# Optimization experiments

Hardware: AMD Instinct MI355X
Metric: run time of the kernel (lower is better)

## Reference

```python
import jax, jax.numpy as jnp
import numpy as np

NUM_USERS = 80000
NUM_ITEMS = 40000
NUM_NODES = NUM_USERS + NUM_ITEMS
LATENT_DIM = 64
N_LAYERS = 3
ALPHA = 0.8
E_POS = 3_000_000
E_NEG = 1_500_000
E_PATH = 2_000_000
N_PATHS = 6


def _make_edges(rng, n_edges, n_nodes):
    # sample keys, dedupe so COO is coalesced (distinct (row,col) pairs)
    keys = rng.integers(0, n_nodes * n_nodes, size=int(n_edges * 1.05), dtype=np.int64)
    keys = np.unique(keys)[:n_edges]
    assert keys.shape[0] == n_edges
    row = (keys // n_nodes).astype(np.int32)
    col = (keys % n_nodes).astype(np.int32)
    return row, col


def setup_inputs() -> dict:
    key = jax.random.key(0)
    k1, k2, k3, k4, k5 = jax.random.split(key, 5)
    rng = np.random.default_rng(0)

    pos_row, pos_col = _make_edges(rng, E_POS, NUM_NODES)
    neg_row, neg_col = _make_edges(rng, E_NEG, NUM_NODES)
    p_row, p_col = _make_edges(rng, E_PATH, NUM_NODES)

    # path membership counts: for each coalesced edge, how many times each of the
    # 6 path matrices contains it (0/1 here); at least one path per edge
    counts = (rng.random((E_PATH, N_PATHS)) < 0.5).astype(np.float32)
    empty = counts.sum(axis=1) == 0
    counts[empty, 0] = 1.0

    return {
        "user_emb": 0.1 * jax.random.normal(k1, (NUM_USERS, LATENT_DIM), jnp.float32),
        "item_emb": 0.1 * jax.random.normal(k2, (NUM_ITEMS, LATENT_DIM), jnp.float32),
        "theta": jnp.ones((N_PATHS,), jnp.float32) / N_PATHS,
        "pos_row": jnp.asarray(pos_row),
        "pos_col": jnp.asarray(pos_col),
        "pos_val": jax.random.uniform(k3, (E_POS,), jnp.float32, 0.01, 1.0),
        "neg_row": jnp.asarray(neg_row),
        "neg_col": jnp.asarray(neg_col),
        "neg_val": jax.random.uniform(k4, (E_NEG,), jnp.float32, 0.01, 1.0),
        "p_row": jnp.asarray(p_row),
        "p_col": jnp.asarray(p_col),
        "p_counts": jnp.asarray(counts),
    }


def _spmm(row, col, val, x, n_nodes):
    # y = A @ x with A given as COO edge list: gather + segment scatter-add
    return jax.ops.segment_sum(val[:, None] * x[col], row, num_segments=n_nodes)


def reference(user_emb, item_emb, theta, pos_row, pos_col, pos_val,
              neg_row, neg_col, neg_val, p_row, p_col, p_counts):
    n = NUM_NODES

    # ---- build path-weighted matrix (coalesce + sparse row softmax, eq.(2)) ----
    theta_w = jax.nn.softmax(theta)                 # [6]
    vals = p_counts @ theta_w                       # coalesced values per edge [E_path]
    exp_v = jnp.exp(vals)
    row_sums = jax.ops.segment_sum(exp_v, p_row, num_segments=n)
    soft_v = exp_v / (row_sums[p_row] + 1e-12)      # row-level sparse softmax

    # ---- PEE: E_0 = P @ all_emb ----
    all_emb = jnp.concatenate([user_emb, item_emb], axis=0)  # [N, D]
    e = _spmm(p_row, p_col, soft_v, all_emb, n)
    embs = [e]

    # ---- signed propagation ----
    for _ in range(N_LAYERS):
        e_pos = _spmm(pos_row, pos_col, pos_val, e, n)
        e_neg_a = _spmm(neg_row, neg_col, neg_val, e, n)
        e = e_pos + ALPHA * (e - e_neg_a)
        embs.append(e)

    light_out = jnp.mean(jnp.stack(embs, axis=1), axis=1)   # [N, D]
    users = light_out[:NUM_USERS]
    items = light_out[NUM_USERS:]
    return users, items
```

## Files before the change

kernel.cpp:

```cpp
#include <hip/hip_runtime.h>

#define NUM_USERS 80000
#define NUM_ITEMS 40000
#define NUM_NODES 120000
#define DIM 64
#define ALPHA_C 0.8f

typedef unsigned short u16;
typedef unsigned int u32;

__device__ __forceinline__ u16 f2bf(float f) {
    union { float f; u32 i; } v;
    v.f = f;
    u32 i = v.i;
    u32 r = (i + 0x7FFFu + ((i >> 16) & 1u)) >> 16;
    return (u16)r;
}
__device__ __forceinline__ float lo_bf(u32 u) { return __uint_as_float(u << 16); }
__device__ __forceinline__ float hi_bf(u32 u) { return __uint_as_float(u & 0xffff0000u); }

__device__ __forceinline__ void acc8(float* __restrict__ acc, float v, uint4 q) {
    const u32* p = (const u32*)&q;
#pragma unroll
    for (int k = 0; k < 4; ++k) {
        u32 u = p[k];
        acc[2 * k]     = fmaf(v, lo_bf(u), acc[2 * k]);
        acc[2 * k + 1] = fmaf(v, hi_bf(u), acc[2 * k + 1]);
    }
}

__device__ __forceinline__ uint4 ldrow(const u16* __restrict__ x, int c, int li) {
    return *((const uint4*)(x + (size_t)c * DIM) + li);
}

__device__ __forceinline__ void seg_pipe(const int* __restrict__ col,
                                         const float* __restrict__ val,
                                         int start, int end,
                                         const u16* __restrict__ x,
                                         int li, float* __restrict__ acc) {
    int n = end - start;
    const int* cp = col + start;
    const float* vp = val + start;
    int np = n >> 1;
    if (np >= 2) {
        int   ca0 = cp[0], ca1 = cp[1];
        float va0 = vp[0], va1 = vp[1];
        int   cb0 = cp[2], cb1 = cp[3];
        float vb0 = vp[2], vb1 = vp[3];
        uint4 xa0 = ldrow(x, ca0, li);
        uint4 xa1 = ldrow(x, ca1, li);
        for (int p = 2; p < np; ++p) {
            int   cc0 = cp[2 * p],     cc1 = cp[2 * p + 1];
            float vc0 = vp[2 * p],     vc1 = vp[2 * p + 1];
            uint4 xb0 = ldrow(x, cb0, li);
            uint4 xb1 = ldrow(x, cb1, li);
            acc8(acc, va0, xa0);
            acc8(acc, va1, xa1);
            va0 = vb0; va1 = vb1; xa0 = xb0; xa1 = xb1;
            cb0 = cc0; cb1 = cc1; vb0 = vc0; vb1 = vc1;
        }
        uint4 xb0 = ldrow(x, cb0, li);
        uint4 xb1 = ldrow(x, cb1, li);
        acc8(acc, va0, xa0);
        acc8(acc, va1, xa1);
        acc8(acc, vb0, xb0);
        acc8(acc, vb1, xb1);
        if (n & 1) {
            int c = cp[n - 1];
            float v = vp[n - 1];
            uint4 xq = ldrow(x, c, li);
            acc8(acc, v, xq);
        }
    } else {
        for (int e = 0; e < n; ++e) {
            int c = cp[e];
            float v = vp[e];
            uint4 xq = ldrow(x, c, li);
            acc8(acc, v, xq);
        }
    }
}

__global__ void k_softmax_theta(const float* __restrict__ theta,
                                float* __restrict__ theta_w) {
    if (threadIdx.x == 0 && blockIdx.x == 0) {
        float m = -1e30f;
        for (int i = 0; i < 6; ++i) m = fmaxf(m, theta[i]);
        float e[6];
        float s = 0.f;
        for (int i = 0; i < 6; ++i) { e[i] = expf(theta[i] - m); s += e[i]; }
        for (int i = 0; i < 6; ++i) theta_w[i] = e[i] / s;
    }
}

__global__ void k_expv(const float* __restrict__ p_counts,
                       const float* __restrict__ theta_w,
                       float* __restrict__ exp_v, int E) {
    int i = blockIdx.x * blockDim.x + threadIdx.x;
    if (i >= E) return;
    const float* c = p_counts + (size_t)i * 6;
    float v = c[0] * theta_w[0] + c[1] * theta_w[1] + c[2] * theta_w[2] +
              c[3] * theta_w[3] + c[4] * theta_w[4] + c[5] * theta_w[5];
    exp_v[i] = expf(v);
}

__device__ __forceinline__ void lower_bound_ptr(const int* __restrict__ rows,
                                                int nnz, int r,
                                                int* __restrict__ ptr) {
    int lo = 0, hi = nnz;
    while (lo < hi) {
        int mid = (lo + hi) >> 1;
        if (rows[mid] < r) lo = mid + 1; else hi = mid;
    }
    ptr[r] = lo;
}

__global__ void k_row_ptr3(const int* __restrict__ rows_a, int nnz_a, int* __restrict__ pa,
                           const int* __restrict__ rows_b, int nnz_b, int* __restrict__ pb,
                           const int* __restrict__ rows_c, int nnz_c, int* __restrict__ pc) {
    int t = blockIdx.x * blockDim.x + threadIdx.x;
    int which = t / (NUM_NODES + 1);
    int r = t - which * (NUM_NODES + 1);
    if (which == 0) lower_bound_ptr(rows_a, nnz_a, r, pa);
    else if (which == 1) lower_bound_ptr(rows_b, nnz_b, r, pb);
    else if (which == 2) lower_bound_ptr(rows_c, nnz_c, r, pc);
}

__global__ void k_cvt(const float* __restrict__ user_emb,
                      const float* __restrict__ item_emb,
                      u16* __restrict__ emb16) {
    int i = blockIdx.x * blockDim.x + threadIdx.x;
    size_t f = (size_t)i * 4;
    const size_t UTOT = (size_t)NUM_USERS * DIM;
    const size_t TOT = (size_t)NUM_NODES * DIM;
    if (f >= TOT) return;
    float4 v = (f < UTOT) ? *(const float4*)(user_emb + f)
                          : *(const float4*)(item_emb + (f - UTOT));
    ushort4 o;
    o.x = f2bf(v.x); o.y = f2bf(v.y); o.z = f2bf(v.z); o.w = f2bf(v.w);
    *(ushort4*)(emb16 + f) = o;
}

__global__ void k_path(const u16* __restrict__ emb16,
                       const float* __restrict__ exp_v,
                       const int* __restrict__ rp,
                       const int* __restrict__ cols,
                       u16* __restrict__ e0,
                       float* __restrict__ sum_out) {
    int t = blockIdx.x * blockDim.x + threadIdx.x;
    int row = t >> 3;
    if (row >= NUM_NODES) return;
    int li = threadIdx.x & 7;
    int start = rp[row], end = rp[row + 1];

    float s = 0.f;
    for (int e = start + li; e < end; e += 8) s += exp_v[e];
    s += __shfl_xor(s, 1);
    s += __shfl_xor(s, 2);
    s += __shfl_xor(s, 4);
    float inv = 1.0f / (s + 1e-12f);

    float acc[8];
#pragma unroll
    for (int k = 0; k < 8; ++k) acc[k] = 0.f;

    seg_pipe(cols, exp_v, start, end, emb16, li, acc);

#pragma unroll
    for (int k = 0; k < 8; ++k) acc[k] *= inv;

    u32 o[4];
#pragma unroll
    for (int k = 0; k < 4; ++k)
        o[k] = (u32)f2bf(acc[2 * k]) | ((u32)f2bf(acc[2 * k + 1]) << 16);
    *((uint4*)(e0 + (size_t)row * DIM) + li) = *(uint4*)o;
    float4* sp = (float4*)(sum_out + (size_t)row * DIM) + li * 2;
    sp[0] = make_float4(acc[0], acc[1], acc[2], acc[3]);
    sp[1] = make_float4(acc[4], acc[5], acc[6], acc[7]);
}

__global__ void k_layer(const u16* __restrict__ e_in,
                        u16* __restrict__ e_out,
                        float* __restrict__ sum_io,
                        const int* __restrict__ rp_p,
                        const int* __restrict__ col_p,
                        const float* __restrict__ val_p,
                        const int* __restrict__ rp_n,
                        const int* __restrict__ col_n,
                        const float* __restrict__ val_n,
                        int is_final) {
    int t = blockIdx.x * blockDim.x + threadIdx.x;
    int row = t >> 3;
    if (row >= NUM_NODES) return;
    int li = threadIdx.x & 7;

    float accp[8], accn[8];
#pragma unroll
    for (int k = 0; k < 8; ++k) { accp[k] = 0.f; accn[k] = 0.f; }

    seg_pipe(col_p, val_p, rp_p[row], rp_p[row + 1], e_in, li, accp);
    seg_pipe(col_n, val_n, rp_n[row], rp_n[row + 1], e_in, li, accn);

    uint4 eq = *((const uint4*)(e_in + (size_t)row * DIM) + li);
    const u32* ep = (const u32*)&eq;
    float res[8];
#pragma unroll
    for (int k = 0; k < 4; ++k) {
        res[2 * k]     = accp[2 * k]     + ALPHA_C * (lo_bf(ep[k]) - accn[2 * k]);
        res[2 * k + 1] = accp[2 * k + 1] + ALPHA_C * (hi_bf(ep[k]) - accn[2 * k + 1]);
    }
    float4* sp = (float4*)(sum_io + (size_t)row * DIM) + li * 2;
    float4 s0 = sp[0], s1 = sp[1];
    s0.x += res[0]; s0.y += res[1]; s0.z += res[2]; s0.w += res[3];
    s1.x += res[4]; s1.y += res[5]; s1.z += res[6]; s1.w += res[7];
    if (is_final) {
        s0.x *= 0.25f; s0.y *= 0.25f; s0.z *= 0.25f; s0.w *= 0.25f;
        s1.x *= 0.25f; s1.y *= 0.25f; s1.z *= 0.25f; s1.w *= 0.25f;
    }
    sp[0] = s0; sp[1] = s1;
    if (!is_final) {
        u32 o[4];
#pragma unroll
        for (int k = 0; k < 4; ++k)
            o[k] = (u32)f2bf(res[2 * k]) | ((u32)f2bf(res[2 * k + 1]) << 16);
        *((uint4*)(e_out + (size_t)row * DIM) + li) = *(uint4*)o;
    }
}

extern "C" void kernel_launch(void* const* d_in, const int* in_sizes, int n_in,
                              void* d_out, int out_size, void* d_ws, size_t ws_size,
                              hipStream_t stream) {
    const float* user_emb = (const float*)d_in[0];
    const float* item_emb = (const float*)d_in[1];
    const float* theta    = (const float*)d_in[2];
    const int*   pos_row  = (const int*)d_in[3];
    const int*   pos_col  = (const int*)d_in[4];
    const float* pos_val  = (const float*)d_in[5];
    const int*   neg_row  = (const int*)d_in[6];
    const int*   neg_col  = (const int*)d_in[7];
    const float* neg_val  = (const float*)d_in[8];
    const int*   p_row    = (const int*)d_in[9];
    const int*   p_col    = (const int*)d_in[10];
    const float* p_counts = (const float*)d_in[11];
    const int E_pos  = in_sizes[3];
    const int E_neg  = in_sizes[6];
    const int E_path = in_sizes[9];

    char* wsb = (char*)d_ws;
    size_t off = 0;
    auto alloc = [&](size_t bytes) -> void* {
        void* p = wsb + off;
        off = (off + bytes + 255) & ~(size_t)255;
        return p;
    };
    float* theta_w = (float*)alloc(6 * sizeof(float));
    float* exp_v   = (float*)alloc((size_t)E_path * sizeof(float));
    int*   rp_pos  = (int*)alloc((size_t)(NUM_NODES + 1) * sizeof(int));
    int*   rp_neg  = (int*)alloc((size_t)(NUM_NODES + 1) * sizeof(int));
    int*   rp_path = (int*)alloc((size_t)(NUM_NODES + 1) * sizeof(int));
    u16*   emb16   = (u16*)alloc((size_t)NUM_NODES * DIM * sizeof(u16));
    u16*   eA      = (u16*)alloc((size_t)NUM_NODES * DIM * sizeof(u16));
    u16*   eB      = (u16*)alloc((size_t)NUM_NODES * DIM * sizeof(u16));
    float* sum_io  = (float*)d_out;

    k_softmax_theta<<<1, 64, 0, stream>>>(theta, theta_w);
    k_expv<<<(E_path + 255) / 256, 256, 0, stream>>>(p_counts, theta_w, exp_v, E_path);

    int total_rp = 3 * (NUM_NODES + 1);
    k_row_ptr3<<<(total_rp + 255) / 256, 256, 0, stream>>>(
        pos_row, E_pos, rp_pos, neg_row, E_neg, rp_neg, p_row, E_path, rp_path);

    int cvt_threads = (NUM_NODES * DIM) / 4;
    k_cvt<<<(cvt_threads + 255) / 256, 256, 0, stream>>>(user_emb, item_emb, emb16);

    int row_blocks = (NUM_NODES + 31) / 32;

    k_path<<<row_blocks, 256, 0, stream>>>(emb16, exp_v, rp_path, p_col, eA, sum_io);
    k_layer<<<row_blocks, 256, 0, stream>>>(eA, eB, sum_io,
                                            rp_pos, pos_col, pos_val,
                                            rp_neg, neg_col, neg_val, 0);
    k_layer<<<row_blocks, 256, 0, stream>>>(eB, eA, sum_io,
                                            rp_pos, pos_col, pos_val,
                                            rp_neg, neg_col, neg_val, 0);
    k_layer<<<row_blocks, 256, 0, stream>>>(eA, eB, sum_io,
                                            rp_pos, pos_col, pos_val,
                                            rp_neg, neg_col, neg_val, 1);
}
```

Before: 477.7 us.

## Merge pos/neg CSR into one pre-scaled edge list; compute path row sums via atomics

Builds a merged CSR for each row: positive edges first, then negative edges with values pre-scaled by -alpha. Each propagation layer then runs a single segmented gather loop instead of two, which cuts per-row overhead and load-latency stalls. The path row softmax denominators are now accumulated with atomics in the exp kernel rather than by a separate pass in k_path. In exchange it adds a merge kernel and extra workspace for the merged arrays, plus atomic contention and a small nondeterminism in summation order.

Measured after the change: 619.9 us. 1.3x slower.

```diff
diff --git a/kernel.cpp b/kernel.cpp
--- a/kernel.cpp
+++ b/kernel.cpp
@@ -95,13 +95,17 @@
 
 __global__ void k_expv(const float* __restrict__ p_counts,
                        const float* __restrict__ theta_w,
-                       float* __restrict__ exp_v, int E) {
+                       const int* __restrict__ p_row,
+                       float* __restrict__ exp_v,
+                       float* __restrict__ row_sum, int E) {
     int i = blockIdx.x * blockDim.x + threadIdx.x;
     if (i >= E) return;
     const float* c = p_counts + (size_t)i * 6;
     float v = c[0] * theta_w[0] + c[1] * theta_w[1] + c[2] * theta_w[2] +
               c[3] * theta_w[3] + c[4] * theta_w[4] + c[5] * theta_w[5];
-    exp_v[i] = expf(v);
+    float ev = expf(v);
+    exp_v[i] = ev;
+    atomicAdd(&row_sum[p_row[i]], ev);
 }
 
 __device__ __forceinline__ void lower_bound_ptr(const int* __restrict__ rows,
@@ -141,8 +145,31 @@
     *(ushort4*)(emb16 + f) = o;
 }
 
+__global__ void k_merge(const int* __restrict__ pos_row, const int* __restrict__ pos_col,
+                        const float* __restrict__ pos_val, int E_pos,
+                        const int* __restrict__ neg_row, const int* __restrict__ neg_col,
+                        const float* __restrict__ neg_val, int E_neg,
+                        const int* __restrict__ rp_p, const int* __restrict__ rp_n,
+                        int* __restrict__ m_col, float* __restrict__ m_val) {
+    int i = blockIdx.x * blockDim.x + threadIdx.x;
+    if (i < E_pos) {
+        int r = pos_row[i];
+        int d = i + rp_n[r];
+        m_col[d] = pos_col[i];
+        m_val[d] = pos_val[i];
+    } else {
+        int j = i - E_pos;
+        if (j >= E_neg) return;
+        int r = neg_row[j];
+        int d = rp_p[r + 1] + j;
+        m_col[d] = neg_col[j];
+        m_val[d] = -ALPHA_C * neg_val[j];
+    }
+}
+
 __global__ void k_path(const u16* __restrict__ emb16,
                        const float* __restrict__ exp_v,
+                       const float* __restrict__ row_sum,
                        const int* __restrict__ rp,
                        const int* __restrict__ cols,
                        u16* __restrict__ e0,
@@ -152,13 +179,7 @@
     if (row >= NUM_NODES) return;
     int li = threadIdx.x & 7;
     int start = rp[row], end = rp[row + 1];
-
-    float s = 0.f;
-    for (int e = start + li; e < end; e += 8) s += exp_v[e];
-    s += __shfl_xor(s, 1);
-    s += __shfl_xor(s, 2);
-    s += __shfl_xor(s, 4);
-    float inv = 1.0f / (s + 1e-12f);
+    float inv = 1.0f / (row_sum[row] + 1e-12f);
 
     float acc[8];
 #pragma unroll
@@ -183,31 +204,31 @@
                         u16* __restrict__ e_out,
                         float* __restrict__ sum_io,
                         const int* __restrict__ rp_p,
-                        const int* __restrict__ col_p,
-                        const float* __restrict__ val_p,
                         const int* __restrict__ rp_n,
-                        const int* __restrict__ col_n,
-                        const float* __restrict__ val_n,
+                        const int* __restrict__ m_col,
+                        const float* __restrict__ m_val,
                         int is_final) {
     int t = blockIdx.x * blockDim.x + threadIdx.x;
     int row = t >> 3;
     if (row >= NUM_NODES) return;
     int li = threadIdx.x & 7;
-
-    float accp[8], accn[8];
-#pragma unroll
-    for (int k = 0; k < 8; ++k) { accp[k] = 0.f; accn[k] = 0.f; }
-
-    seg_pipe(col_p, val_p, rp_p[row], rp_p[row + 1], e_in, li, accp);
-    seg_pipe(col_n, val_n, rp_n[row], rp_n[row + 1], e_in, li, accn);
+    int start = rp_p[row] + rp_n[row];
+    int end   = rp_p[row + 1] + rp_n[row + 1];
 
     uint4 eq = *((const uint4*)(e_in + (size_t)row * DIM) + li);
+
+    float acc[8];
+#pragma unroll
+    for (int k = 0; k < 8; ++k) acc[k] = 0.f;
+
+    seg_pipe(m_col, m_val, start, end, e_in, li, acc);
+
     const u32* ep = (const u32*)&eq;
     float res[8];
 #pragma unroll
     for (int k = 0; k < 4; ++k) {
-        res[2 * k]     = accp[2 * k]     + ALPHA_C * (lo_bf(ep[k]) - accn[2 * k]);
-        res[2 * k + 1] = accp[2 * k + 1] + ALPHA_C * (hi_bf(ep[k]) - accn[2 * k + 1]);
+        res[2 * k]     = acc[2 * k]     + ALPHA_C * lo_bf(ep[k]);
+        res[2 * k + 1] = acc[2 * k + 1] + ALPHA_C * hi_bf(ep[k]);
     }
     float4* sp = (float4*)(sum_io + (size_t)row * DIM) + li * 2;
     float4 s0 = sp[0], s1 = sp[1];
@@ -255,16 +276,22 @@
     };
     float* theta_w = (float*)alloc(6 * sizeof(float));
     float* exp_v   = (float*)alloc((size_t)E_path * sizeof(float));
+    float* row_sum = (float*)alloc((size_t)NUM_NODES * sizeof(float));
     int*   rp_pos  = (int*)alloc((size_t)(NUM_NODES + 1) * sizeof(int));
     int*   rp_neg  = (int*)alloc((size_t)(NUM_NODES + 1) * sizeof(int));
     int*   rp_path = (int*)alloc((size_t)(NUM_NODES + 1) * sizeof(int));
     u16*   emb16   = (u16*)alloc((size_t)NUM_NODES * DIM * sizeof(u16));
     u16*   eA      = (u16*)alloc((size_t)NUM_NODES * DIM * sizeof(u16));
     u16*   eB      = (u16*)alloc((size_t)NUM_NODES * DIM * sizeof(u16));
+    int*   m_col   = (int*)alloc((size_t)(E_pos + E_neg) * sizeof(int));
+    float* m_val   = (float*)alloc((size_t)(E_pos + E_neg) * sizeof(float));
     float* sum_io  = (float*)d_out;
 
+    hipMemsetAsync(row_sum, 0, (size_t)NUM_NODES * sizeof(float), stream);
+
     k_softmax_theta<<<1, 64, 0, stream>>>(theta, theta_w);
-    k_expv<<<(E_path + 255) / 256, 256, 0, stream>>>(p_counts, theta_w, exp_v, E_path);
+    k_expv<<<(E_path + 255) / 256, 256, 0, stream>>>(p_counts, theta_w, p_row,
+                                                     exp_v, row_sum, E_path);
 
     int total_rp = 3 * (NUM_NODES + 1);
     k_row_ptr3<<<(total_rp + 255) / 256, 256, 0, stream>>>(
@@ -273,16 +300,20 @@
     int cvt_threads = (NUM_NODES * DIM) / 4;
     k_cvt<<<(cvt_threads + 255) / 256, 256, 0, stream>>>(user_emb, item_emb, emb16);
 
+    int merge_threads = E_pos + E_neg;
+    k_merge<<<(merge_threads + 255) / 256, 256, 0, stream>>>(
+        pos_row, pos_col, pos_val, E_pos,
+        neg_row, neg_col, neg_val, E_neg,
+        rp_pos, rp_neg, m_col, m_val);
+
     int row_blocks = (NUM_NODES + 31) / 32;
 
-    k_path<<<row_blocks, 256, 0, stream>>>(emb16, exp_v, rp_path, p_col, eA, sum_io);
-    k_layer<<<row_blocks, 256, 0, stream>>>(eA, eB, sum_io,
-                                            rp_pos, pos_col, pos_val,
-                                            rp_neg, neg_col, neg_val, 0);
-    k_layer<<<row_blocks, 256, 0, stream>>>(eB, eA, sum_io,
-                                            rp_pos, pos_col, pos_val,
-                                            rp_neg, neg_col, neg_val, 0);
-    k_layer<<<row_blocks, 256, 0, stream>>>(eA, eB, sum_io,
-                                            rp_pos, pos_col, pos_val,
-                                            rp_neg, neg_col, neg_val, 1);
-}
+    k_path<<<row_blocks, 256, 0, stream>>>(emb16, exp_v, row_sum, rp_path,
+                                           p_col, eA, sum_io);
+    k_layer<<<row_blocks, 256, 0, stream>>>(eA, eB, sum_io, rp_pos, rp_neg,
+                                            m_col, m_val, 0);
+    k_layer<<<row_blocks, 256, 0, stream>>>(eB, eA, sum_io, rp_pos, rp_neg,
+                                            m_col, m_val, 0);
+    k_layer<<<row_blocks, 256, 0, stream>>>(eA, eB, sum_io, rp_pos, rp_neg,
+                                            m_col, m_val, 1);
+}
```

## Drop fp32 running sum, keep bf16 layer outputs and average in final layer

Applied to the files above, without the earlier changes.

The fp32 running-sum buffer that every layer read and wrote is removed. Each layer's bf16 output is now kept in its own buffer, and the final layer reads e0 and e1 to compute the mean, writing fp32 output once. The path kernel folds the row exp-sum into the gather loop instead of doing a separate strided pass, and the layer kernel uses a single accumulator with the negative edges scaled by -alpha. This cuts per-layer fp32 traffic and register use. The cost is that the mean is now taken over bf16-rounded intermediates rather than fp32 ones, with an extra buffer allocated.

New measurement: 461.6 us. 1.03x faster.

```diff
diff --git a/kernel.cpp b/kernel.cpp
--- a/kernel.cpp
+++ b/kernel.cpp
@@ -33,52 +33,58 @@
     return *((const uint4*)(x + (size_t)c * DIM) + li);
 }
 
-__device__ __forceinline__ void seg_pipe(const int* __restrict__ col,
-                                         const float* __restrict__ val,
-                                         int start, int end,
-                                         const u16* __restrict__ x,
-                                         int li, float* __restrict__ acc) {
+template <bool SUMV>
+__device__ __forceinline__ void seg_pipe_t(const int* __restrict__ col,
+                                           const float* __restrict__ val,
+                                           int start, int end,
+                                           const u16* __restrict__ x,
+                                           int li, float scale,
+                                           float* __restrict__ acc,
+                                           float* __restrict__ vsum) {
     int n = end - start;
     const int* cp = col + start;
     const float* vp = val + start;
+    float s = 0.f;
     int np = n >> 1;
     if (np >= 2) {
-        int   ca0 = cp[0], ca1 = cp[1];
         float va0 = vp[0], va1 = vp[1];
         int   cb0 = cp[2], cb1 = cp[3];
         float vb0 = vp[2], vb1 = vp[3];
-        uint4 xa0 = ldrow(x, ca0, li);
-        uint4 xa1 = ldrow(x, ca1, li);
+        uint4 xa0 = ldrow(x, cp[0], li);
+        uint4 xa1 = ldrow(x, cp[1], li);
         for (int p = 2; p < np; ++p) {
             int   cc0 = cp[2 * p],     cc1 = cp[2 * p + 1];
             float vc0 = vp[2 * p],     vc1 = vp[2 * p + 1];
             uint4 xb0 = ldrow(x, cb0, li);
             uint4 xb1 = ldrow(x, cb1, li);
-            acc8(acc, va0, xa0);
-            acc8(acc, va1, xa1);
+            acc8(acc, va0 * scale, xa0);
+            acc8(acc, va1 * scale, xa1);
+            if (SUMV) s += va0 + va1;
             va0 = vb0; va1 = vb1; xa0 = xb0; xa1 = xb1;
             cb0 = cc0; cb1 = cc1; vb0 = vc0; vb1 = vc1;
         }
         uint4 xb0 = ldrow(x, cb0, li);
         uint4 xb1 = ldrow(x, cb1, li);
-        acc8(acc, va0, xa0);
-        acc8(acc, va1, xa1);
-        acc8(acc, vb0, xb0);
-        acc8(acc, vb1, xb1);
+        acc8(acc, va0 * scale, xa0);
+        acc8(acc, va1 * scale, xa1);
+        acc8(acc, vb0 * scale, xb0);
+        acc8(acc, vb1 * scale, xb1);
+        if (SUMV) s += va0 + va1 + vb0 + vb1;
         if (n & 1) {
-            int c = cp[n - 1];
             float v = vp[n - 1];
-            uint4 xq = ldrow(x, c, li);
-            acc8(acc, v, xq);
+            uint4 xq = ldrow(x, cp[n - 1], li);
+            acc8(acc, v * scale, xq);
+            if (SUMV) s += v;
         }
     } else {
         for (int e = 0; e < n; ++e) {
-            int c = cp[e];
             float v = vp[e];
-            uint4 xq = ldrow(x, c, li);
-            acc8(acc, v, xq);
-        }
-    }
+            uint4 xq = ldrow(x, cp[e], li);
+            acc8(acc, v * scale, xq);
+            if (SUMV) s += v;
+        }
+    }
+    if (SUMV) *vsum = s;
 }
 
 __global__ void k_softmax_theta(const float* __restrict__ theta,
@@ -145,80 +151,82 @@
                        const float* __restrict__ exp_v,
                        const int* __restrict__ rp,
                        const int* __restrict__ cols,
-                       u16* __restrict__ e0,
-                       float* __restrict__ sum_out) {
+                       u16* __restrict__ e0) {
     int t = blockIdx.x * blockDim.x + threadIdx.x;
     int row = t >> 3;
     if (row >= NUM_NODES) return;
     int li = threadIdx.x & 7;
     int start = rp[row], end = rp[row + 1];
 
+    float acc[8];
+#pragma unroll
+    for (int k = 0; k < 8; ++k) acc[k] = 0.f;
     float s = 0.f;
-    for (int e = start + li; e < end; e += 8) s += exp_v[e];
-    s += __shfl_xor(s, 1);
-    s += __shfl_xor(s, 2);
-    s += __shfl_xor(s, 4);
+
+    seg_pipe_t<true>(cols, exp_v, start, end, emb16, li, 1.0f, acc, &s);
+
     float inv = 1.0f / (s + 1e-12f);
-
-    float acc[8];
-#pragma unroll
-    for (int k = 0; k < 8; ++k) acc[k] = 0.f;
-
-    seg_pipe(cols, exp_v, start, end, emb16, li, acc);
-
-#pragma unroll
-    for (int k = 0; k < 8; ++k) acc[k] *= inv;
-
     u32 o[4];
 #pragma unroll
     for (int k = 0; k < 4; ++k)
-        o[k] = (u32)f2bf(acc[2 * k]) | ((u32)f2bf(acc[2 * k + 1]) << 16);
+        o[k] = (u32)f2bf(acc[2 * k] * inv) | ((u32)f2bf(acc[2 * k + 1] * inv) << 16);
     *((uint4*)(e0 + (size_t)row * DIM) + li) = *(uint4*)o;
-    float4* sp = (float4*)(sum_out + (size_t)row * DIM) + li * 2;
-    sp[0] = make_float4(acc[0], acc[1], acc[2], acc[3]);
-    sp[1] = make_float4(acc[4], acc[5], acc[6], acc[7]);
-}
-
-__global__ void k_layer(const u16* __restrict__ e_in,
-                        u16* __restrict__ e_out,
-                        float* __restrict__ sum_io,
-                        const int* __restrict__ rp_p,
-                        const int* __restrict__ col_p,
-                        const float* __restrict__ val_p,
-                        const int* __restrict__ rp_n,
-                        const int* __restrict__ col_n,
-                        const float* __restrict__ val_n,
-                        int is_final) {
+}
+
+template <int FINAL>
+__global__ void k_layer_t(const u16* __restrict__ e_in,
+                          u16* __restrict__ e_out,
+                          const u16* __restrict__ e0,
+                          const u16* __restrict__ e1,
+                          float* __restrict__ out,
+                          const int* __restrict__ rp_p,
+                          const int* __restrict__ col_p,
+                          const float* __restrict__ val_p,
+                          const int* __restrict__ rp_n,
+                          const int* __restrict__ col_n,
+                          const float* __restrict__ val_n) {
     int t = blockIdx.x * blockDim.x + threadIdx.x;
     int row = t >> 3;
     if (row >= NUM_NODES) return;
     int li = threadIdx.x & 7;
 
-    float accp[8], accn[8];
-#pragma unroll
-    for (int k = 0; k < 8; ++k) { accp[k] = 0.f; accn[k] = 0.f; }
-
-    seg_pipe(col_p, val_p, rp_p[row], rp_p[row + 1], e_in, li, accp);
-    seg_pipe(col_n, val_n, rp_n[row], rp_n[row + 1], e_in, li, accn);
-
     uint4 eq = *((const uint4*)(e_in + (size_t)row * DIM) + li);
+
+    float acc[8];
+#pragma unroll
+    for (int k = 0; k < 8; ++k) acc[k] = 0.f;
+
+    seg_pipe_t<false>(col_p, val_p, rp_p[row], rp_p[row + 1], e_in, li, 1.0f,
+                      acc, nullptr);
+    seg_pipe_t<false>(col_n, val_n, rp_n[row], rp_n[row + 1], e_in, li, -ALPHA_C,
+                      acc, nullptr);
+
     const u32* ep = (const u32*)&eq;
     float res[8];
 #pragma unroll
     for (int k = 0; k < 4; ++k) {
-        res[2 * k]     = accp[2 * k]     + ALPHA_C * (lo_bf(ep[k]) - accn[2 * k]);
-        res[2 * k + 1] = accp[2 * k + 1] + ALPHA_C * (hi_bf(ep[k]) - accn[2 * k + 1]);
-    }
-    float4* sp = (float4*)(sum_io + (size_t)row * DIM) + li * 2;
-    float4 s0 = sp[0], s1 = sp[1];
-    s0.x += res[0]; s0.y += res[1]; s0.z += res[2]; s0.w += res[3];
-    s1.x += res[4]; s1.y += res[5]; s1.z += res[6]; s1.w += res[7];
-    if (is_final) {
-        s0.x *= 0.25f; s0.y *= 0.25f; s0.z *= 0.25f; s0.w *= 0.25f;
-        s1.x *= 0.25f; s1.y *= 0.25f; s1.z *= 0.25f; s1.w *= 0.25f;
-    }
-    sp[0] = s0; sp[1] = s1;
-    if (!is_final) {
+        res[2 * k]     = acc[2 * k]     + ALPHA_C * lo_bf(ep[k]);
+        res[2 * k + 1] = acc[2 * k + 1] + ALPHA_C * hi_bf(ep[k]);
+    }
+
+    if (FINAL) {
+        uint4 q0 = *((const uint4*)(e0 + (size_t)row * DIM) + li);
+        uint4 q1 = *((const uint4*)(e1 + (size_t)row * DIM) + li);
+        const u32* p0 = (const u32*)&q0;
+        const u32* p1 = (const u32*)&q1;
+        float4 o0, o1;
+        float* oo[2] = { (float*)&o0, (float*)&o1 };
+#pragma unroll
+        for (int k = 0; k < 4; ++k) {
+            float lo = res[2 * k]     + lo_bf(ep[k]) + lo_bf(p0[k]) + lo_bf(p1[k]);
+            float hi = res[2 * k + 1] + hi_bf(ep[k]) + hi_bf(p0[k]) + hi_bf(p1[k]);
+            oo[k >> 1][(k & 1) * 2]     = 0.25f * lo;
+            oo[k >> 1][(k & 1) * 2 + 1] = 0.25f * hi;
+        }
+        float4* sp = (float4*)(out + (size_t)row * DIM) + li * 2;
+        sp[0] = o0;
+        sp[1] = o1;
+    } else {
         u32 o[4];
 #pragma unroll
         for (int k = 0; k < 4; ++k)
@@ -259,9 +267,10 @@
     int*   rp_neg  = (int*)alloc((size_t)(NUM_NODES + 1) * sizeof(int));
     int*   rp_path = (int*)alloc((size_t)(NUM_NODES + 1) * sizeof(int));
     u16*   emb16   = (u16*)alloc((size_t)NUM_NODES * DIM * sizeof(u16));
-    u16*   eA      = (u16*)alloc((size_t)NUM_NODES * DIM * sizeof(u16));
-    u16*   eB      = (u16*)alloc((size_t)NUM_NODES * DIM * sizeof(u16));
-    float* sum_io  = (float*)d_out;
+    u16*   e0      = (u16*)alloc((size_t)NUM_NODES * DIM * sizeof(u16));
+    u16*   e1      = (u16*)alloc((size_t)NUM_NODES * DIM * sizeof(u16));
+    u16*   e2      = (u16*)alloc((size_t)NUM_NODES * DIM * sizeof(u16));
+    float* outp    = (float*)d_out;
 
     k_softmax_theta<<<1, 64, 0, stream>>>(theta, theta_w);
     k_expv<<<(E_path + 255) / 256, 256, 0, stream>>>(p_counts, theta_w, exp_v, E_path);
@@ -275,14 +284,14 @@
 
     int row_blocks = (NUM_NODES + 31) / 32;
 
-    k_path<<<row_blocks, 256, 0, stream>>>(emb16, exp_v, rp_path, p_col, eA, sum_io);
-    k_layer<<<row_blocks, 256, 0, stream>>>(eA, eB, sum_io,
-                                            rp_pos, pos_col, pos_val,
-                                            rp_neg, neg_col, neg_val, 0);
-    k_layer<<<row_blocks, 256, 0, stream>>>(eB, eA, sum_io,
-                                            rp_pos, pos_col, pos_val,
-                                            rp_neg, neg_col, neg_val, 0);
-    k_layer<<<row_blocks, 256, 0, stream>>>(eA, eB, sum_io,
-                                            rp_pos, pos_col, pos_val,
-                                            rp_neg, neg_col, neg_val, 1);
-}
+    k_path<<<row_blocks, 256, 0, stream>>>(emb16, exp_v, rp_path, p_col, e0);
+    k_layer_t<0><<<row_blocks, 256, 0, stream>>>(e0, e1, nullptr, nullptr, nullptr,
+                                                 rp_pos, pos_col, pos_val,
+                                                 rp_neg, neg_col, neg_val);
+    k_layer_t<0><<<row_blocks, 256, 0, stream>>>(e1, e2, nullptr, nullptr, nullptr,
+                                                 rp_pos, pos_col, pos_val,
+                                                 rp_neg, neg_col, neg_val);
+    k_layer_t<1><<<row_blocks, 256, 0, stream>>>(e2, nullptr, e0, e1, outp,
+                                                 rp_pos, pos_col, pos_val,
+                                                 rp_neg, neg_col, neg_val);
+}
```
